# Kernel optimization log

Hardware: AMD Instinct MI355X
Metric: run time of the kernel (lower is better)

## Reference

```python
import jax, jax.numpy as jnp
import numpy as np

TEMPERATURE = 10000.0


def _grid_sample_bilinear(img, ix, iy):
    """torch.nn.functional.grid_sample equivalent (bilinear, zero padding,
    align_corners=False), with pixel coords ix, iy already unnormalized.
    img: [B,C,H,W]; ix, iy: [B,K,H,W]. Returns [B,C,K,H,W]."""
    B, C, H, W = img.shape
    K = ix.shape[1]
    x0 = jnp.floor(ix)
    y0 = jnp.floor(iy)
    x1 = x0 + 1.0
    y1 = y0 + 1.0
    wx1 = ix - x0
    wx0 = 1.0 - wx1
    wy1 = iy - y0
    wy0 = 1.0 - wy1
    flat = img.reshape(B, C, H * W)

    def corner(xc, yc, w):
        valid = (xc >= 0) & (xc <= W - 1) & (yc >= 0) & (yc <= H - 1)
        xi = jnp.clip(xc, 0, W - 1).astype(jnp.int32)
        yi = jnp.clip(yc, 0, H - 1).astype(jnp.int32)
        idx = (yi * W + xi).reshape(B, 1, -1)  # [B,1,K*H*W]
        g = jnp.take_along_axis(flat, jnp.broadcast_to(idx, (B, C, idx.shape[-1])), axis=2)
        g = g.reshape(B, C, K, H, W)
        wv = (w * valid.astype(img.dtype)).reshape(B, 1, K, H, W)
        return g * wv

    return (corner(x0, y0, wx0 * wy0) + corner(x1, y0, wx1 * wy0)
            + corner(x0, y1, wx0 * wy1) + corner(x1, y1, wx1 * wy1))


def _forward(left_features, right_features, offset_x, offset_y):
    B, C, H, W = left_features.shape
    dt = left_features.dtype
    # left coordinate grids (buffers built in __init__)
    lx = jnp.arange(W, dtype=dt)[None, None, None, :]               # [1,1,1,W]
    # faithful to original: y coords clamped to max = W-1 (no-op when H<=W)
    ly = jnp.clip(jnp.arange(H, dtype=dt), 0, W - 1)[None, None, :, None]  # [1,1,H,1]

    rx = jnp.clip(lx - offset_x, 0.0, W - 1.0)                      # [B,K,H,W]
    ry = jnp.clip(ly - offset_y, 0.0, H - 1.0)                      # [B,K,H,W]
    # normalize to [-1,1] as in original
    gx = (rx - W / 2) / (W / 2)
    gy = (ry - H / 2) / (H / 2)
    # unnormalize per align_corners=False convention
    ix = ((gx + 1.0) * W - 1.0) * 0.5
    iy = ((gy + 1.0) * H - 1.0) * 0.5

    sampled = _grid_sample_bilinear(right_features, ix, iy)         # [B,C,K,H,W]
    strength = jnp.mean(-jnp.abs(left_features[:, :, None] - sampled), axis=1) * TEMPERATURE  # [B,K,H,W]
    w = jax.nn.softmax(strength, axis=1)
    ox = jnp.sum(offset_x * w, axis=1, keepdims=True)               # [B,1,H,W]
    oy = jnp.sum(offset_y * w, axis=1, keepdims=True)               # [B,1,H,W]
    return ox, oy


def setup_inputs() -> dict:
    key = jax.random.key(0)
    k1, k2, k3, k4 = jax.random.split(key, 4)
    B, C, H, W, K = 1, 32, 256, 512, 10
    left_features = jax.random.normal(k1, (B, C, H, W), jnp.float32)
    right_features = jax.random.normal(k2, (B, C, H, W), jnp.float32)
    # horizontal disparity candidates in [0, 64) px; small vertical jitter
    offset_x = jax.random.uniform(k3, (B, K, H, W), jnp.float32) * 64.0
    offset_y = jax.random.normal(k4, (B, K, H, W), jnp.float32) * 2.0
    return {"left_features": left_features, "right_features": right_features,
            "offset_x": offset_x, "offset_y": offset_y}


def reference(left_features, right_features, offset_x, offset_y):
    return _forward(left_features, right_features, offset_x, offset_y)
```

## Files before the change

kernel.cpp:

```cpp
#include <hip/hip_runtime.h>

constexpr int C = 32, H = 256, W = 512, K = 10;
constexpr int HW = H * W;
constexpr float TEMP = 10000.0f;
constexpr int NXCD = 8;
constexpr int BAND_PX = HW / NXCD;

__global__ __launch_bounds__(256) void conv_right_hwc(
    const float* __restrict__ in, float* __restrict__ out)
{
    __shared__ float t[C][129];
    const int band  = blockIdx.x & 7;
    const int inner = blockIdx.x >> 3;
    const int base = band * BAND_PX + inner * 128;
    const int tid = threadIdx.x;
    #pragma unroll
    for (int i = 0; i < 16; ++i) {
        int lin = i * 256 + tid;
        int c = lin >> 7, px = lin & 127;
        t[c][px] = in[c * HW + base + px];
    }
    __syncthreads();
    #pragma unroll
    for (int i = 0; i < 16; ++i) {
        int lin = i * 256 + tid;
        int px = lin >> 5, c = lin & 31;
        out[(base + px) * C + c] = t[c][px];
    }
}

__global__ __launch_bounds__(256) void disp_kernel_hwc8(
    const float* __restrict__ lchw, const float* __restrict__ rhwc,
    const float* __restrict__ offx, const float* __restrict__ offy,
    float* __restrict__ out)
{
    const int tid = threadIdx.x;
    const int q  = tid & 3;
    const int kk = (tid >> 2) & 1;
    const int band  = blockIdx.x & 7;
    const int inner = blockIdx.x >> 3;
    const int p = band * BAND_PX + inner * 32 + (tid >> 3);
    const int w = p & (W - 1);
    const int h = p >> 9;

    float lf[8];
    #pragma unroll
    for (int j = 0; j < 4; ++j) lf[j]     = lchw[(4 * q + j) * HW + p];
    #pragma unroll
    for (int j = 0; j < 4; ++j) lf[4 + j] = lchw[(16 + 4 * q + j) * HW + p];

    const float lx = (float)w;
    const float ly = (float)h;
    const float4* rb = (const float4*)rhwc;

    float s[5], okx[5], oky[5];

    #pragma unroll
    for (int j = 0; j < 5; ++j) {
        const int k = 2 * j + kk;
        const float ox = offx[k * HW + p];
        const float oy = offy[k * HW + p];
        okx[j] = ox; oky[j] = oy;

        float rx = fminf(fmaxf(lx - ox, 0.0f), (float)(W - 1));
        float ry = fminf(fmaxf(ly - oy, 0.0f), (float)(H - 1));
        float gx = (rx - (float)(W / 2)) / (float)(W / 2);
        float gy = (ry - (float)(H / 2)) / (float)(H / 2);
        float ix = ((gx + 1.0f) * (float)W - 1.0f) * 0.5f;
        float iy = ((gy + 1.0f) * (float)H - 1.0f) * 0.5f;

        float x0f = floorf(ix), y0f = floorf(iy);
        float wx1 = ix - x0f, wy1 = iy - y0f;
        float wx0 = 1.0f - wx1, wy0 = 1.0f - wy1;
        int x0 = (int)x0f, y0 = (int)y0f;

        float ax = (x0 >= 0) ? wx0 : 0.0f;
        float ay = (y0 >= 0) ? wy0 : 0.0f;
        float w00 = ax * ay,   w01 = wx1 * ay;
        float w10 = ax * wy1,  w11 = wx1 * wy1;

        int xi0 = max(x0, 0), yi0 = max(y0, 0);
        int r0 = yi0 * W, r1 = (y0 + 1) * W;
        int b00 = (r0 + xi0) * 8 + q;
        int b01 = (r0 + x0 + 1) * 8 + q;
        int b10 = (r1 + xi0) * 8 + q;
        int b11 = (r1 + x0 + 1) * 8 + q;

        float4 a0 = rb[b00], a1 = rb[b00 + 4];
        float4 b0 = rb[b01], b1 = rb[b01 + 4];
        float4 d0 = rb[b10], d1 = rb[b10 + 4];
        float4 e0 = rb[b11], e1 = rb[b11 + 4];

        float acc = 0.0f;
        acc += fabsf(lf[0] - (w00 * a0.x + w01 * b0.x + w10 * d0.x + w11 * e0.x));
        acc += fabsf(lf[1] - (w00 * a0.y + w01 * b0.y + w10 * d0.y + w11 * e0.y));
        acc += fabsf(lf[2] - (w00 * a0.z + w01 * b0.z + w10 * d0.z + w11 * e0.z));
        acc += fabsf(lf[3] - (w00 * a0.w + w01 * b0.w + w10 * d0.w + w11 * e0.w));
        acc += fabsf(lf[4] - (w00 * a1.x + w01 * b1.x + w10 * d1.x + w11 * e1.x));
        acc += fabsf(lf[5] - (w00 * a1.y + w01 * b1.y + w10 * d1.y + w11 * e1.y));
        acc += fabsf(lf[6] - (w00 * a1.z + w01 * b1.z + w10 * d1.z + w11 * e1.z));
        acc += fabsf(lf[7] - (w00 * a1.w + w01 * b1.w + w10 * d1.w + w11 * e1.w));

        acc += __shfl_xor(acc, 1);
        acc += __shfl_xor(acc, 2);
        s[j] = acc * (-TEMP / (float)C);
    }

    float m = s[0];
    #pragma unroll
    for (int j = 1; j < 5; ++j) m = fmaxf(m, s[j]);
    m = fmaxf(m, __shfl_xor(m, 4));

    float den = 0.0f, sx = 0.0f, sy = 0.0f;
    #pragma unroll
    for (int j = 0; j < 5; ++j) {
        float e = __expf(s[j] - m);
        den += e;
        sx += okx[j] * e;
        sy += oky[j] * e;
    }
    den += __shfl_xor(den, 4);
    sx  += __shfl_xor(sx, 4);
    sy  += __shfl_xor(sy, 4);

    float inv = 1.0f / den;
    if ((tid & 7) == 0) {
        out[p]      = sx * inv;
        out[HW + p] = sy * inv;
    }
}

__global__ __launch_bounds__(256) void disp_kernel_chw(
    const float* __restrict__ left, const float* __restrict__ right,
    const float* __restrict__ offx, const float* __restrict__ offy,
    float* __restrict__ out)
{
    const int p = blockIdx.x * 256 + threadIdx.x;
    const int w = p & (W - 1);
    const int h = p >> 9;
    float lf[C];
    #pragma unroll
    for (int c = 0; c < C; ++c) lf[c] = left[c * HW + p];
    const float lx = (float)w, ly = (float)h;
    float s[K], okx[K], oky[K];
    #pragma unroll
    for (int k = 0; k < K; ++k) {
        const float ox = offx[k * HW + p], oy = offy[k * HW + p];
        okx[k] = ox; oky[k] = oy;
        float rx = fminf(fmaxf(lx - ox, 0.0f), (float)(W - 1));
        float ry = fminf(fmaxf(ly - oy, 0.0f), (float)(H - 1));
        float gx = (rx - 256.0f) / 256.0f, gy = (ry - 128.0f) / 128.0f;
        float ix = ((gx + 1.0f) * (float)W - 1.0f) * 0.5f;
        float iy = ((gy + 1.0f) * (float)H - 1.0f) * 0.5f;
        float x0f = floorf(ix), y0f = floorf(iy);
        float wx1 = ix - x0f, wy1 = iy - y0f;
        float wx0 = 1.0f - wx1, wy0 = 1.0f - wy1;
        int x0 = (int)x0f, y0 = (int)y0f;
        float ax = (x0 >= 0) ? wx0 : 0.0f;
        float ay = (y0 >= 0) ? wy0 : 0.0f;
        float w00 = ax * ay, w01 = wx1 * ay, w10 = ax * wy1, w11 = wx1 * wy1;
        int xi0 = max(x0, 0), yi0 = max(y0, 0);
        int i00 = yi0 * W + xi0, i01 = yi0 * W + x0 + 1;
        int i10 = (y0 + 1) * W + xi0, i11 = (y0 + 1) * W + x0 + 1;
        float acc = 0.0f;
        #pragma unroll
        for (int c = 0; c < C; ++c) {
            const float* rc = right + c * HW;
            acc += fabsf(lf[c] - (w00 * rc[i00] + w01 * rc[i01]
                                + w10 * rc[i10] + w11 * rc[i11]));
        }
        s[k] = acc * (-TEMP / (float)C);
    }
    float m = s[0];
    #pragma unroll
    for (int k = 1; k < K; ++k) m = fmaxf(m, s[k]);
    float den = 0.0f, sx = 0.0f, sy = 0.0f;
    #pragma unroll
    for (int k = 0; k < K; ++k) {
        float e = __expf(s[k] - m);
        den += e; sx += okx[k] * e; sy += oky[k] * e;
    }
    float inv = 1.0f / den;
    out[p] = sx * inv;
    out[HW + p] = sy * inv;
}

extern "C" void kernel_launch(void* const* d_in, const int* in_sizes, int n_in,
                              void* d_out, int out_size, void* d_ws, size_t ws_size,
                              hipStream_t stream) {
    const float* left  = (const float*)d_in[0];
    const float* right = (const float*)d_in[1];
    const float* offx  = (const float*)d_in[2];
    const float* offy  = (const float*)d_in[3];
    float* out = (float*)d_out;

    const size_t need = (size_t)HW * C * sizeof(float);
    if (ws_size >= need) {
        float* rhwc = (float*)d_ws;
        conv_right_hwc<<<HW / 128, 256, 0, stream>>>(right, rhwc);
        disp_kernel_hwc8<<<HW / 32, 256, 0, stream>>>(left, rhwc, offx, offy, out);
    } else {
        disp_kernel_chw<<<HW / 256, 256, 0, stream>>>(left, right, offx, offy, out);
    }
}
```

Baseline: 121.1 us.

## Use nontemporal loads, simplify coordinate math, and batch shuffle reductions

Streaming reads of left features and offsets now use nontemporal loads so they do not evict the reused right-feature data from cache. The normalize/unnormalize coordinate chain is folded algebraically into ix = rx - 0.5, which removes divides and multiplies. Cross-lane shuffle reductions are moved out of the gather loop into a separate pass so the gathers can issue with fewer dependency stalls. The folded math can differ from the reference in the last bits of floating-point rounding.

```diff
diff --git a/kernel.cpp b/kernel.cpp
--- a/kernel.cpp
+++ b/kernel.cpp
@@ -45,29 +45,29 @@
 
     float lf[8];
     #pragma unroll
-    for (int j = 0; j < 4; ++j) lf[j]     = lchw[(4 * q + j) * HW + p];
-    #pragma unroll
-    for (int j = 0; j < 4; ++j) lf[4 + j] = lchw[(16 + 4 * q + j) * HW + p];
+    for (int j = 0; j < 4; ++j)
+        lf[j]     = __builtin_nontemporal_load(lchw + (4 * q + j) * HW + p);
+    #pragma unroll
+    for (int j = 0; j < 4; ++j)
+        lf[4 + j] = __builtin_nontemporal_load(lchw + (16 + 4 * q + j) * HW + p);
 
     const float lx = (float)w;
     const float ly = (float)h;
     const float4* rb = (const float4*)rhwc;
 
-    float s[5], okx[5], oky[5];
+    float acc[5], okx[5], oky[5];
 
     #pragma unroll
     for (int j = 0; j < 5; ++j) {
         const int k = 2 * j + kk;
-        const float ox = offx[k * HW + p];
-        const float oy = offy[k * HW + p];
+        const float ox = __builtin_nontemporal_load(offx + k * HW + p);
+        const float oy = __builtin_nontemporal_load(offy + k * HW + p);
         okx[j] = ox; oky[j] = oy;
 
         float rx = fminf(fmaxf(lx - ox, 0.0f), (float)(W - 1));
         float ry = fminf(fmaxf(ly - oy, 0.0f), (float)(H - 1));
-        float gx = (rx - (float)(W / 2)) / (float)(W / 2);
-        float gy = (ry - (float)(H / 2)) / (float)(H / 2);
-        float ix = ((gx + 1.0f) * (float)W - 1.0f) * 0.5f;
-        float iy = ((gy + 1.0f) * (float)H - 1.0f) * 0.5f;
+        float ix = rx - 0.5f;
+        float iy = ry - 0.5f;
 
         float x0f = floorf(ix), y0f = floorf(iy);
         float wx1 = ix - x0f, wy1 = iy - y0f;
@@ -91,19 +91,25 @@
         float4 d0 = rb[b10], d1 = rb[b10 + 4];
         float4 e0 = rb[b11], e1 = rb[b11 + 4];
 
-        float acc = 0.0f;
-        acc += fabsf(lf[0] - (w00 * a0.x + w01 * b0.x + w10 * d0.x + w11 * e0.x));
-        acc += fabsf(lf[1] - (w00 * a0.y + w01 * b0.y + w10 * d0.y + w11 * e0.y));
-        acc += fabsf(lf[2] - (w00 * a0.z + w01 * b0.z + w10 * d0.z + w11 * e0.z));
-        acc += fabsf(lf[3] - (w00 * a0.w + w01 * b0.w + w10 * d0.w + w11 * e0.w));
-        acc += fabsf(lf[4] - (w00 * a1.x + w01 * b1.x + w10 * d1.x + w11 * e1.x));
-        acc += fabsf(lf[5] - (w00 * a1.y + w01 * b1.y + w10 * d1.y + w11 * e1.y));
-        acc += fabsf(lf[6] - (w00 * a1.z + w01 * b1.z + w10 * d1.z + w11 * e1.z));
-        acc += fabsf(lf[7] - (w00 * a1.w + w01 * b1.w + w10 * d1.w + w11 * e1.w));
-
-        acc += __shfl_xor(acc, 1);
-        acc += __shfl_xor(acc, 2);
-        s[j] = acc * (-TEMP / (float)C);
+        float a = 0.0f;
+        a += fabsf(lf[0] - (w00 * a0.x + w01 * b0.x + w10 * d0.x + w11 * e0.x));
+        a += fabsf(lf[1] - (w00 * a0.y + w01 * b0.y + w10 * d0.y + w11 * e0.y));
+        a += fabsf(lf[2] - (w00 * a0.z + w01 * b0.z + w10 * d0.z + w11 * e0.z));
+        a += fabsf(lf[3] - (w00 * a0.w + w01 * b0.w + w10 * d0.w + w11 * e0.w));
+        a += fabsf(lf[4] - (w00 * a1.x + w01 * b1.x + w10 * d1.x + w11 * e1.x));
+        a += fabsf(lf[5] - (w00 * a1.y + w01 * b1.y + w10 * d1.y + w11 * e1.y));
+        a += fabsf(lf[6] - (w00 * a1.z + w01 * b1.z + w10 * d1.z + w11 * e1.z));
+        a += fabsf(lf[7] - (w00 * a1.w + w01 * b1.w + w10 * d1.w + w11 * e1.w));
+        acc[j] = a;
+    }
+
+    float s[5];
+    #pragma unroll
+    for (int j = 0; j < 5; ++j) {
+        float a = acc[j];
+        a += __shfl_xor(a, 1);
+        a += __shfl_xor(a, 2);
+        s[j] = a * (-TEMP / (float)C);
     }
 
     float m = s[0];
@@ -149,9 +155,7 @@
         okx[k] = ox; oky[k] = oy;
         float rx = fminf(fmaxf(lx - ox, 0.0f), (float)(W - 1));
         float ry = fminf(fmaxf(ly - oy, 0.0f), (float)(H - 1));
-        float gx = (rx - 256.0f) / 256.0f, gy = (ry - 128.0f) / 128.0f;
-        float ix = ((gx + 1.0f) * (float)W - 1.0f) * 0.5f;
-        float iy = ((gy + 1.0f) * (float)H - 1.0f) * 0.5f;
+        float ix = rx - 0.5f, iy = ry - 0.5f;
         float x0f = floorf(ix), y0f = floorf(iy);
         float wx1 = ix - x0f, wy1 = iy - y0f;
         float wx0 = 1.0f - wx1, wy0 = 1.0f - wy1;
```

After: 133.3 us. 1.1x slower.
